# Kernel optimization log

Hardware: AMD Instinct MI355X
Metric: run time of the kernel (lower is better)

Reference implementation:

```python
import jax, jax.numpy as jnp
import numpy as np

N = 9                      # qubits (fixed by ExactQCNN9Open)
DIM = 2 ** N               # 512
SQ2 = 1.0 / np.sqrt(2.0)
T_PH = np.complex64(np.exp(1j * np.pi / 4))   # T-gate phase
TD_PH = np.conj(T_PH)                          # Tdg phase

# State layout follows torchquantum: shape (bsz, 2,2,...,2), wire w on axis w+1
# (wire 0 is the most-significant bit of the flat 512-dim index).

def _h(s, w):
    s = jnp.moveaxis(s, w + 1, 1)
    s = jnp.stack([s[:, 0] + s[:, 1], s[:, 0] - s[:, 1]], axis=1) * SQ2
    return jnp.moveaxis(s, 1, w + 1)

def _phase(s, w, ph):  # diag(1, ph) on wire w
    s = jnp.moveaxis(s, w + 1, 1)
    s = s.at[:, 1].multiply(ph)
    return jnp.moveaxis(s, 1, w + 1)

def _cz(s, a, b):
    s = jnp.moveaxis(s, (a + 1, b + 1), (1, 2))
    s = s.at[:, 1, 1].multiply(-1.0)
    return jnp.moveaxis(s, (1, 2), (a + 1, b + 1))

def _cnot(s, c, t):
    s = jnp.moveaxis(s, (c + 1, t + 1), (1, 2))
    s = s.at[:, 1].set(s[:, 1, ::-1])  # flip target where control=1
    return jnp.moveaxis(s, (1, 2), (c + 1, t + 1))

def _swap(s, a, b):
    return jnp.swapaxes(s, a + 1, b + 1)

def _toffoli_dec(s, c1, c2, t):
    s = _h(s, t)
    s = _cnot(s, c2, t); s = _phase(s, t, TD_PH)
    s = _cnot(s, c1, t); s = _phase(s, t, T_PH)
    s = _cnot(s, c2, t); s = _phase(s, t, TD_PH)
    s = _cnot(s, c1, t)
    s = _phase(s, c2, T_PH); s = _phase(s, t, T_PH)
    s = _cnot(s, c1, c2)
    s = _h(s, t)
    s = _phase(s, c1, T_PH); s = _phase(s, c2, TD_PH)
    s = _cnot(s, c1, c2)
    return s

def _toffoli_x_controls(s, c1, c2, t):
    s = _h(s, c1); s = _h(s, c2)
    s = _toffoli_dec(s, c1, c2, t)
    s = _h(s, c1); s = _h(s, c2)
    return s

def _circuit(psi):  # psi: (bsz, 512) complex64
    s = psi.reshape((psi.shape[0],) + (2,) * N)
    # --- convolution layer ---
    for i in range(0, N - 1, 2):
        s = _cz(s, i, i + 1)
    for i in range(1, N - 1, 2):
        s = _cz(s, i, i + 1)
    s = _cz(s, 1, 4); s = _cz(s, 4, 7)           # kept-wire CZs
    for (left, mid, right) in [(0, 1, 2), (3, 4, 5), (6, 7, 8)]:
        s = _toffoli_x_controls(s, left, right, mid)
    for i in range(2, N - 1, 3):                 # i = 2, 5
        s = _swap(s, i, i + 1)
    # --- pooling layer ---
    for i in range(0, N - 1, 3):                 # i = 0, 3, 6
        s = _h(s, i); s = _cz(s, i, i + 1)
    for i in range(2, N, 3):                     # i = 2, 5, 8
        s = _h(s, i); s = _cz(s, i, i - 1)
    # --- fc layer ---
    s = _cz(s, 1, 4); s = _cz(s, 4, 7)
    return s

def _expval_x(s, w):  # <psi| X_w |psi>, real-valued, shape (bsz,)
    sx = jnp.flip(s, axis=w + 1)
    return jnp.real(jnp.sum(jnp.conj(s) * sx, axis=tuple(range(1, N + 1))))


def setup_inputs() -> dict:
    key = jax.random.key(0)
    k1, k2 = jax.random.split(key)
    bsz = 65536
    sr = jax.random.normal(k1, (bsz, DIM), dtype=jnp.float32)
    si = jax.random.normal(k2, (bsz, DIM), dtype=jnp.float32)
    # normalize each state vector (valid quantum states)
    norm = jnp.sqrt(jnp.sum(sr * sr + si * si, axis=-1, keepdims=True))
    sr = sr / norm
    si = si / norm
    return {"states_real": sr, "states_imag": si, "n_shots": 0}


def reference(states_real, states_imag, n_shots):
    # n_shots <= 0 -> analytical expectation (the n_shots=None branch)
    psi = (states_real + 1j * states_imag).astype(jnp.complex64)
    s = _circuit(psi)
    return _expval_x(s, 4)  # readout wire = kept[1] = 4
```

## Files before the change

### kernel.cpp

```cpp
#include <hip/hip_runtime.h>

#define DIM 512

__device__ __forceinline__ float sgnf(int par) {
    return __int_as_float(0x3F800000u | ((unsigned)par << 31));
}

__global__ __launch_bounds__(256) void qcnn9_kernel(
    const float* __restrict__ sr, const float* __restrict__ si,
    float* __restrict__ out, int bsz)
{
    const int tid   = blockIdx.x * blockDim.x + threadIdx.x;
    const int state = tid >> 6;
    const int lane  = threadIdx.x & 63;
    if (state >= bsz) return;

    const float* __restrict__ pr = sr + (size_t)state * DIM + lane * 8;
    const float* __restrict__ pi = si + (size_t)state * DIM + lane * 8;

    float zr[8], zi[8];
    {
        float4 r0 = *reinterpret_cast<const float4*>(pr);
        float4 r1 = *reinterpret_cast<const float4*>(pr + 4);
        float4 i0 = *reinterpret_cast<const float4*>(pi);
        float4 i1 = *reinterpret_cast<const float4*>(pi + 4);
        zr[0]=r0.x; zr[1]=r0.y; zr[2]=r0.z; zr[3]=r0.w;
        zr[4]=r1.x; zr[5]=r1.y; zr[6]=r1.z; zr[7]=r1.w;
        zi[0]=i0.x; zi[1]=i0.y; zi[2]=i0.z; zi[3]=i0.w;
        zi[4]=i1.x; zi[5]=i1.y; zi[6]=i1.z; zi[7]=i1.w;
    }

    const int base = lane * 8;

    #pragma unroll
    for (int j = 0; j < 8; ++j) {
        int idx = base + j;
        int t = idx & (idx >> 1);
        int u = idx & (idx >> 3);
        int par = __popc((t & 0xFF) | ((u & 0x12) << 8)) & 1;
        float s = sgnf(par);
        zr[j] *= s; zi[j] *= s;
    }

    #pragma unroll
    for (int b = 0; b < 3; ++b) {
        const int m = 1 << b;
        #pragma unroll
        for (int j = 0; j < 8; ++j) {
            if (!(j & m)) {
                const int k = j | m;
                float ar = zr[j], ai = zi[j];
                float br = zr[k], bi = zi[k];
                zr[j] = ar + br; zi[j] = ai + bi;
                zr[k] = ar - br; zi[k] = ai - bi;
            }
        }
    }

    #pragma unroll
    for (int b = 0; b < 6; ++b) {
        const int m = 1 << b;
        const float s = (lane & m) ? -1.0f : 1.0f;
        #pragma unroll
        for (int j = 0; j < 8; ++j) {
            float tr = __shfl_xor(zr[j], m, 64);
            float ti = __shfl_xor(zi[j], m, 64);
            zr[j] = fmaf(s, zr[j], tr);
            zi[j] = fmaf(s, zi[j], ti);
        }
    }

    float acc = 0.0f;
    #pragma unroll
    for (int j = 0; j < 8; ++j) {
        float prr = __shfl_xor(zr[j ^ 2], 16, 64);
        float pii = __shfl_xor(zi[j ^ 2], 16, 64);
        int idx = base + j;
        int par = ((idx >> 6) ^ (idx >> 4) ^ (idx >> 2)
                   ^ ((idx >> 8) & (idx >> 6))
                   ^ (idx & (idx >> 2))) & 1;
        float s = sgnf(par);
        float term = fmaf(zr[j], prr, zi[j] * pii);
        acc = fmaf(s, term, acc);
    }

    #pragma unroll
    for (int m = 32; m >= 1; m >>= 1)
        acc += __shfl_xor(acc, m, 64);

    if (lane == 0) out[state] = acc * (1.0f / 512.0f);
}

extern "C" void kernel_launch(void* const* d_in, const int* in_sizes, int n_in,
                              void* d_out, int out_size, void* d_ws, size_t ws_size,
                              hipStream_t stream) {
    const float* sr = (const float*)d_in[0];
    const float* si = (const float*)d_in[1];
    float* out = (float*)d_out;
    const int bsz = in_sizes[0] / DIM;

    const int threads = 256;
    const int blocks  = (bsz * 64 + threads - 1) / threads;
    qcnn9_kernel<<<blocks, threads, 0, stream>>>(sr, si, out, bsz);
}
```

Baseline: 285.6 us.

## Process two states per wave and use DPP/swizzle for cross-lane butterflies

Each wavefront now handles two state vectors, doubling the independent work per lane so memory latency and cross-lane operations can overlap. Generic shfl_xor (ds_bpermute) is replaced by DPP quad moves for xor 1/2 and ds_swizzle for xor 4/8/16, leaving bpermute only for xor 32. The cost is higher register pressure and half as many waves. Since the kernel reads 268 MB of input, it is likely memory-bound, so the gain may be limited.

```diff
diff --git a/kernel.cpp b/kernel.cpp
--- a/kernel.cpp
+++ b/kernel.cpp
@@ -6,29 +6,42 @@
     return __int_as_float(0x3F800000u | ((unsigned)par << 31));
 }
 
+template<int PAT>
+__device__ __forceinline__ float swz(float x) {
+    return __int_as_float(__builtin_amdgcn_ds_swizzle(__float_as_int(x), PAT));
+}
+template<int CTRL>
+__device__ __forceinline__ float dppmov(float x) {
+    return __int_as_float(__builtin_amdgcn_mov_dpp(__float_as_int(x), CTRL, 0xF, 0xF, true));
+}
+__device__ __forceinline__ float sx32(float x) { return __shfl_xor(x, 32, 64); }
+
 __global__ __launch_bounds__(256) void qcnn9_kernel(
     const float* __restrict__ sr, const float* __restrict__ si,
     float* __restrict__ out, int bsz)
 {
-    const int tid   = blockIdx.x * blockDim.x + threadIdx.x;
-    const int state = tid >> 6;
-    const int lane  = threadIdx.x & 63;
-    if (state >= bsz) return;
+    const int wid  = (blockIdx.x * blockDim.x + threadIdx.x) >> 6;
+    const int lane = threadIdx.x & 63;
+    const int s0   = wid * 2;
+    if (s0 >= bsz) return;
+    const bool hasB = (s0 + 1) < bsz;
 
-    const float* __restrict__ pr = sr + (size_t)state * DIM + lane * 8;
-    const float* __restrict__ pi = si + (size_t)state * DIM + lane * 8;
+    const size_t offA = (size_t)s0 * DIM + lane * 8;
+    const size_t offB = offA + (hasB ? DIM : 0);
 
-    float zr[8], zi[8];
-    {
-        float4 r0 = *reinterpret_cast<const float4*>(pr);
-        float4 r1 = *reinterpret_cast<const float4*>(pr + 4);
-        float4 i0 = *reinterpret_cast<const float4*>(pi);
-        float4 i1 = *reinterpret_cast<const float4*>(pi + 4);
-        zr[0]=r0.x; zr[1]=r0.y; zr[2]=r0.z; zr[3]=r0.w;
-        zr[4]=r1.x; zr[5]=r1.y; zr[6]=r1.z; zr[7]=r1.w;
-        zi[0]=i0.x; zi[1]=i0.y; zi[2]=i0.z; zi[3]=i0.w;
-        zi[4]=i1.x; zi[5]=i1.y; zi[6]=i1.z; zi[7]=i1.w;
-    }
+    float4 ar0 = *reinterpret_cast<const float4*>(sr + offA);
+    float4 ar1 = *reinterpret_cast<const float4*>(sr + offA + 4);
+    float4 ai0 = *reinterpret_cast<const float4*>(si + offA);
+    float4 ai1 = *reinterpret_cast<const float4*>(si + offA + 4);
+    float4 br0 = *reinterpret_cast<const float4*>(sr + offB);
+    float4 br1 = *reinterpret_cast<const float4*>(sr + offB + 4);
+    float4 bi0 = *reinterpret_cast<const float4*>(si + offB);
+    float4 bi1 = *reinterpret_cast<const float4*>(si + offB + 4);
+
+    float z0r[8] = {ar0.x,ar0.y,ar0.z,ar0.w, ar1.x,ar1.y,ar1.z,ar1.w};
+    float z0i[8] = {ai0.x,ai0.y,ai0.z,ai0.w, ai1.x,ai1.y,ai1.z,ai1.w};
+    float z1r[8] = {br0.x,br0.y,br0.z,br0.w, br1.x,br1.y,br1.z,br1.w};
+    float z1i[8] = {bi0.x,bi0.y,bi0.z,bi0.w, bi1.x,bi1.y,bi1.z,bi1.w};
 
     const int base = lane * 8;
 
@@ -37,9 +50,8 @@
         int idx = base + j;
         int t = idx & (idx >> 1);
         int u = idx & (idx >> 3);
-        int par = __popc((t & 0xFF) | ((u & 0x12) << 8)) & 1;
-        float s = sgnf(par);
-        zr[j] *= s; zi[j] *= s;
+        float s = sgnf(__popc((t & 0xFF) | ((u & 0x12) << 8)) & 1);
+        z0r[j] *= s; z0i[j] *= s; z1r[j] *= s; z1i[j] *= s;
     }
 
     #pragma unroll
@@ -49,46 +61,65 @@
         for (int j = 0; j < 8; ++j) {
             if (!(j & m)) {
                 const int k = j | m;
-                float ar = zr[j], ai = zi[j];
-                float br = zr[k], bi = zi[k];
-                zr[j] = ar + br; zi[j] = ai + bi;
-                zr[k] = ar - br; zi[k] = ai - bi;
+                float x, y;
+                x = z0r[j]; y = z0r[k]; z0r[j] = x + y; z0r[k] = x - y;
+                x = z0i[j]; y = z0i[k]; z0i[j] = x + y; z0i[k] = x - y;
+                x = z1r[j]; y = z1r[k]; z1r[j] = x + y; z1r[k] = x - y;
+                x = z1i[j]; y = z1i[k]; z1i[j] = x + y; z1i[k] = x - y;
             }
         }
     }
 
-    #pragma unroll
-    for (int b = 0; b < 6; ++b) {
-        const int m = 1 << b;
-        const float s = (lane & m) ? -1.0f : 1.0f;
-        #pragma unroll
-        for (int j = 0; j < 8; ++j) {
-            float tr = __shfl_xor(zr[j], m, 64);
-            float ti = __shfl_xor(zi[j], m, 64);
-            zr[j] = fmaf(s, zr[j], tr);
-            zi[j] = fmaf(s, zi[j], ti);
-        }
+#define XSTAGE(MBIT, XF)                                                      \
+    {                                                                         \
+        const float s = (lane & (MBIT)) ? -1.0f : 1.0f;                       \
+        _Pragma("unroll")                                                     \
+        for (int j = 0; j < 8; ++j) {                                         \
+            float t0r = XF(z0r[j]); float t0i = XF(z0i[j]);                   \
+            float t1r = XF(z1r[j]); float t1i = XF(z1i[j]);                   \
+            z0r[j] = fmaf(s, z0r[j], t0r); z0i[j] = fmaf(s, z0i[j], t0i);     \
+            z1r[j] = fmaf(s, z1r[j], t1r); z1i[j] = fmaf(s, z1i[j], t1i);     \
+        }                                                                     \
     }
+    XSTAGE(1,  dppmov<0xB1>)
+    XSTAGE(2,  dppmov<0x4E>)
+    XSTAGE(4,  swz<0x101F>)
+    XSTAGE(8,  swz<0x201F>)
+    XSTAGE(16, swz<0x401F>)
+    XSTAGE(32, sx32)
+#undef XSTAGE
 
-    float acc = 0.0f;
+    float acc0 = 0.0f, acc1 = 0.0f;
     #pragma unroll
     for (int j = 0; j < 8; ++j) {
-        float prr = __shfl_xor(zr[j ^ 2], 16, 64);
-        float pii = __shfl_xor(zi[j ^ 2], 16, 64);
+        float p0r = swz<0x401F>(z0r[j ^ 2]);
+        float p0i = swz<0x401F>(z0i[j ^ 2]);
+        float p1r = swz<0x401F>(z1r[j ^ 2]);
+        float p1i = swz<0x401F>(z1i[j ^ 2]);
         int idx = base + j;
         int par = ((idx >> 6) ^ (idx >> 4) ^ (idx >> 2)
                    ^ ((idx >> 8) & (idx >> 6))
                    ^ (idx & (idx >> 2))) & 1;
         float s = sgnf(par);
-        float term = fmaf(zr[j], prr, zi[j] * pii);
-        acc = fmaf(s, term, acc);
+        acc0 = fmaf(s, fmaf(z0r[j], p0r, z0i[j] * p0i), acc0);
+        acc1 = fmaf(s, fmaf(z1r[j], p1r, z1i[j] * p1i), acc1);
     }
 
-    #pragma unroll
-    for (int m = 32; m >= 1; m >>= 1)
-        acc += __shfl_xor(acc, m, 64);
+    { float t0 = dppmov<0xB1>(acc0),  t1 = dppmov<0xB1>(acc1);  acc0 += t0; acc1 += t1; }
+    { float t0 = dppmov<0x4E>(acc0),  t1 = dppmov<0x4E>(acc1);  acc0 += t0; acc1 += t1; }
+    { float t0 = swz<0x101F>(acc0),   t1 = swz<0x101F>(acc1);   acc0 += t0; acc1 += t1; }
+    { float t0 = swz<0x201F>(acc0),   t1 = swz<0x201F>(acc1);   acc0 += t0; acc1 += t1; }
+    { float t0 = swz<0x401F>(acc0),   t1 = swz<0x401F>(acc1);   acc0 += t0; acc1 += t1; }
+    { float t0 = sx32(acc0),          t1 = sx32(acc1);          acc0 += t0; acc1 += t1; }
 
-    if (lane == 0) out[state] = acc * (1.0f / 512.0f);
+    if (lane == 0) {
+        if (hasB) {
+            *reinterpret_cast<float2*>(out + s0) =
+                make_float2(acc0 * (1.0f / 512.0f), acc1 * (1.0f / 512.0f));
+        } else {
+            out[s0] = acc0 * (1.0f / 512.0f);
+        }
+    }
 }
 
 extern "C" void kernel_launch(void* const* d_in, const int* in_sizes, int n_in,
@@ -100,6 +131,7 @@
     const int bsz = in_sizes[0] / DIM;
 
     const int threads = 256;
-    const int blocks  = (bsz * 64 + threads - 1) / threads;
+    const int nwaves  = (bsz + 1) / 2;
+    const int blocks  = (nwaves * 64 + threads - 1) / threads;
     qcnn9_kernel<<<blocks, threads, 0, stream>>>(sr, si, out, bsz);
 }
```

Measured after the change: 270.8 us. 5.2% less time.

## Process four states per wavefront with 32 amplitudes per lane and DPP exchanges

Applied to the files above, without the earlier changes.

Each wavefront now handles four state vectors, with 16 lanes per state and 32 contiguous amplitudes per lane. More of the Walsh-Hadamard butterflies run in registers, which removes several cross-lane shuffle stages. The remaining exchanges and the final reduction use DPP moves and ds_swizzle instead of generic shuffles. The sign patterns are folded into precomputed bitmasks, and the final readout pairing becomes register-local. The cost is higher register pressure from 64 floats per lane, which can lower occupancy, and a less coalesced per-lane load pattern.

```diff
diff --git a/kernel.cpp b/kernel.cpp
--- a/kernel.cpp
+++ b/kernel.cpp
@@ -6,89 +6,100 @@
     return __int_as_float(0x3F800000u | ((unsigned)par << 31));
 }
 
+template<int PAT>
+__device__ __forceinline__ float swz(float x) {
+    return __int_as_float(__builtin_amdgcn_ds_swizzle(__float_as_int(x), PAT));
+}
+template<int CTRL>
+__device__ __forceinline__ float dppmov(float x) {
+    return __int_as_float(__builtin_amdgcn_mov_dpp(__float_as_int(x), CTRL, 0xF, 0xF, true));
+}
+
 __global__ __launch_bounds__(256) void qcnn9_kernel(
     const float* __restrict__ sr, const float* __restrict__ si,
     float* __restrict__ out, int bsz)
 {
-    const int tid   = blockIdx.x * blockDim.x + threadIdx.x;
-    const int state = tid >> 6;
+    const int wid   = (blockIdx.x * blockDim.x + threadIdx.x) >> 6;
     const int lane  = threadIdx.x & 63;
-    if (state >= bsz) return;
+    const int g     = lane & 15;
+    const int sIdx  = wid * 4 + (lane >> 4);
+    const int state = min(sIdx, bsz - 1);
 
-    const float* __restrict__ pr = sr + (size_t)state * DIM + lane * 8;
-    const float* __restrict__ pi = si + (size_t)state * DIM + lane * 8;
+    const float* __restrict__ pr = sr + (size_t)state * DIM + g * 32;
+    const float* __restrict__ pi = si + (size_t)state * DIM + g * 32;
 
-    float zr[8], zi[8];
-    {
-        float4 r0 = *reinterpret_cast<const float4*>(pr);
-        float4 r1 = *reinterpret_cast<const float4*>(pr + 4);
-        float4 i0 = *reinterpret_cast<const float4*>(pi);
-        float4 i1 = *reinterpret_cast<const float4*>(pi + 4);
-        zr[0]=r0.x; zr[1]=r0.y; zr[2]=r0.z; zr[3]=r0.w;
-        zr[4]=r1.x; zr[5]=r1.y; zr[6]=r1.z; zr[7]=r1.w;
-        zi[0]=i0.x; zi[1]=i0.y; zi[2]=i0.z; zi[3]=i0.w;
-        zi[4]=i1.x; zi[5]=i1.y; zi[6]=i1.z; zi[7]=i1.w;
+    float vr[32], vi[32];
+    #pragma unroll
+    for (int q = 0; q < 8; ++q) {
+        float4 a = reinterpret_cast<const float4*>(pr)[q];
+        vr[4*q] = a.x; vr[4*q+1] = a.y; vr[4*q+2] = a.z; vr[4*q+3] = a.w;
+    }
+    #pragma unroll
+    for (int q = 0; q < 8; ++q) {
+        float4 a = reinterpret_cast<const float4*>(pi)[q];
+        vi[4*q] = a.x; vi[4*q+1] = a.y; vi[4*q+2] = a.z; vi[4*q+3] = a.w;
     }
 
-    const int base = lane * 8;
+    const int g0 = g & 1, g1 = (g >> 1) & 1, g2 = (g >> 2) & 1, g3 = (g >> 3) & 1;
 
-    #pragma unroll
-    for (int j = 0; j < 8; ++j) {
-        int idx = base + j;
-        int t = idx & (idx >> 1);
-        int u = idx & (idx >> 3);
-        int par = __popc((t & 0xFF) | ((u & 0x12) << 8)) & 1;
-        float s = sgnf(par);
-        zr[j] *= s; zi[j] *= s;
+    {
+        const int B = (g0 & g1) ^ (g1 & g2) ^ (g2 & g3);
+        const int C = g0 ^ g2;
+        unsigned M = 0x8B84B848u ^ (C ? 0xFFFF0000u : 0u) ^ (B ? 0xFFFFFFFFu : 0u);
+        #pragma unroll
+        for (int j = 0; j < 32; ++j) {
+            float s = sgnf((M >> j) & 1);
+            vr[j] *= s; vi[j] *= s;
+        }
     }
 
     #pragma unroll
-    for (int b = 0; b < 3; ++b) {
+    for (int b = 0; b < 5; ++b) {
         const int m = 1 << b;
         #pragma unroll
-        for (int j = 0; j < 8; ++j) {
+        for (int j = 0; j < 32; ++j) {
             if (!(j & m)) {
                 const int k = j | m;
-                float ar = zr[j], ai = zi[j];
-                float br = zr[k], bi = zi[k];
-                zr[j] = ar + br; zi[j] = ai + bi;
-                zr[k] = ar - br; zi[k] = ai - bi;
+                float x, y;
+                x = vr[j]; y = vr[k]; vr[j] = x + y; vr[k] = x - y;
+                x = vi[j]; y = vi[k]; vi[j] = x + y; vi[k] = x - y;
             }
         }
     }
 
-    #pragma unroll
-    for (int b = 0; b < 6; ++b) {
-        const int m = 1 << b;
-        const float s = (lane & m) ? -1.0f : 1.0f;
+#define XSTAGE(MBIT, CTRL)                                                    \
+    {                                                                         \
+        const float s_ = (lane & (MBIT)) ? -1.0f : 1.0f;                      \
+        _Pragma("unroll")                                                     \
+        for (int j = 0; j < 32; ++j) {                                        \
+            float tr = dppmov<CTRL>(vr[j]);                                   \
+            float ti = dppmov<CTRL>(vi[j]);                                   \
+            vr[j] = fmaf(s_, vr[j], tr);                                      \
+            vi[j] = fmaf(s_, vi[j], ti);                                      \
+        }                                                                     \
+    }
+    XSTAGE(1, 0xB1)
+    XSTAGE(2, 0x4E)
+    XSTAGE(8, 0x128)
+#undef XSTAGE
+
+    float acc = 0.0f;
+    {
+        const int SB = (g1 & (g3 ^ 1)) ^ g2;
+        unsigned R = 0xAFAF5050u ^ (SB ? 0xFFFFFFFFu : 0u);
         #pragma unroll
-        for (int j = 0; j < 8; ++j) {
-            float tr = __shfl_xor(zr[j], m, 64);
-            float ti = __shfl_xor(zi[j], m, 64);
-            zr[j] = fmaf(s, zr[j], tr);
-            zi[j] = fmaf(s, zi[j], ti);
+        for (int j = 0; j < 32; ++j) {
+            float p = fmaf(vr[j], vr[j ^ 2], vi[j] * vi[j ^ 2]);
+            acc = fmaf(sgnf((R >> j) & 1), p, acc);
         }
     }
 
-    float acc = 0.0f;
-    #pragma unroll
-    for (int j = 0; j < 8; ++j) {
-        float prr = __shfl_xor(zr[j ^ 2], 16, 64);
-        float pii = __shfl_xor(zi[j ^ 2], 16, 64);
-        int idx = base + j;
-        int par = ((idx >> 6) ^ (idx >> 4) ^ (idx >> 2)
-                   ^ ((idx >> 8) & (idx >> 6))
-                   ^ (idx & (idx >> 2))) & 1;
-        float s = sgnf(par);
-        float term = fmaf(zr[j], prr, zi[j] * pii);
-        acc = fmaf(s, term, acc);
-    }
+    acc += dppmov<0xB1>(acc);
+    acc += dppmov<0x4E>(acc);
+    acc += swz<0x101F>(acc);
+    acc += dppmov<0x128>(acc);
 
-    #pragma unroll
-    for (int m = 32; m >= 1; m >>= 1)
-        acc += __shfl_xor(acc, m, 64);
-
-    if (lane == 0) out[state] = acc * (1.0f / 512.0f);
+    if (g == 0 && sIdx < bsz) out[sIdx] = acc * (1.0f / 256.0f);
 }
 
 extern "C" void kernel_launch(void* const* d_in, const int* in_sizes, int n_in,
@@ -100,6 +111,7 @@
     const int bsz = in_sizes[0] / DIM;
 
     const int threads = 256;
-    const int blocks  = (bsz * 64 + threads - 1) / threads;
+    const int nwaves  = (bsz + 3) / 4;
+    const int blocks  = (nwaves * 64 + threads - 1) / threads;
     qcnn9_kernel<<<blocks, threads, 0, stream>>>(sr, si, out, bsz);
 }
```

After: 280.7 us. About the same (-1.7%).
